# Performance work log

Hardware: AMD Instinct MI355X
Metric: run time of the kernel (lower is better)

The kernel has to match this reference:

```python
import jax, jax.numpy as jnp
import numpy as np

KEEP_RATIO = 0.7  # fully-annealed keep ratio (epoch >= 2*warmup_epochs)


def setup_inputs() -> dict:
    key = jax.random.key(0)
    k0, k1, k2 = jax.random.split(key, 3)
    B, H, W, C, HID = 16, 128, 128, 256, 128
    N = H * W
    tokens = jax.random.normal(k0, (B, N, C), dtype=jnp.float32)
    # xavier_uniform-ish init for the scorer MLP
    lim1 = float(np.sqrt(6.0 / (C + HID)))
    lim2 = float(np.sqrt(6.0 / (HID + 1)))
    w1 = jax.random.uniform(k1, (C, HID), minval=-lim1, maxval=lim1, dtype=jnp.float32)
    b1 = jnp.zeros((HID,), dtype=jnp.float32)
    w2 = jax.random.uniform(k2, (HID, 1), minval=-lim2, maxval=lim2, dtype=jnp.float32)
    b2 = jnp.zeros((1,), dtype=jnp.float32)
    return {"tokens": tokens, "w1": w1, "b1": b1, "w2": w2, "b2": b2}


def reference(tokens, w1, b1, w2, b2):
    # tokens: [B, N, C]; importance scorer: fc1 -> GELU(exact) -> fc2 -> squeeze
    B, N, C = tokens.shape
    num_keep = int(N * KEEP_RATIO)  # static; min_tokens=10 << num_keep
    h = jax.nn.gelu(jnp.einsum("bnc,ch->bnh", tokens, w1) + b1, approximate=False)
    scores = (jnp.einsum("bnh,ho->bno", h, w2) + b2)[..., 0]  # [B, N]
    # top-k token selection, then sort kept indices to preserve spatial order
    _, top_idx = jax.lax.top_k(scores, num_keep)          # [B, K]
    kept_indices = jnp.sort(top_idx, axis=-1)              # [B, K]
    pruned_tokens = jnp.take_along_axis(tokens, kept_indices[..., None], axis=1)  # [B, K, C]
    return pruned_tokens, kept_indices, scores
```

## Files before the change

kernel.cpp:

```cpp
#include <hip/hip_runtime.h>
#include <math.h>

#define B_ 16
#define N_ 16384
#define C_ 256
#define H_ 128
#define K_ 11468
#define G_ ((B_ * N_) / 16)
#define GPB_ 16
#define NBLK_ (G_ / GPB_)

typedef __attribute__((ext_vector_type(8))) short s16x8;
typedef __attribute__((ext_vector_type(4))) float f32x4;
typedef __attribute__((ext_vector_type(4))) unsigned int u32x4;

__device__ __forceinline__ unsigned short f2bf(float f) {
  unsigned u = __builtin_bit_cast(unsigned, f);
  return (unsigned short)((u + 0x7FFFu + ((u >> 16) & 1u)) >> 16);
}
__device__ __forceinline__ unsigned fkey(float f) {
  unsigned u = __builtin_bit_cast(unsigned, f);
  return (u & 0x80000000u) ? ~u : (u | 0x80000000u);
}
__device__ __forceinline__ unsigned pk2(float hi, float lo) {
  return __builtin_amdgcn_perm(__builtin_bit_cast(unsigned, hi),
                               __builtin_bit_cast(unsigned, lo), 0x07060302u);
}

#define LDS_BARRIER()                                     \
  do {                                                    \
    asm volatile("s_waitcnt lgkmcnt(0)" ::: "memory");    \
    __builtin_amdgcn_s_barrier();                         \
  } while (0)

__device__ __forceinline__ float gelu_fast(float h) {
  const float t = 0.5f * h * h;
  const float u = 0.147f * t;
  const float num = t * (1.2732395f + u);
  const float den = 1.0f + u;
  const float r = num * __builtin_amdgcn_rcpf(den);
  const float e = __builtin_amdgcn_exp2f(r * -1.44269504f);
  const float s = __builtin_amdgcn_sqrtf(fmaxf(1.0f - e, 0.0f));
  const unsigned sgn = __builtin_bit_cast(unsigned, h) & 0x80000000u;
  const float erfv = __builtin_bit_cast(float, __builtin_bit_cast(unsigned, s) | sgn);
  return 0.5f * h * (1.0f + erfv);
}

__global__ void k_prep(const float* __restrict__ w1, unsigned short* __restrict__ w1t) {
  int i = blockIdx.x * blockDim.x + threadIdx.x;
  if (i < C_ * H_) {
    int c = i / H_, h = i % H_;
    w1t[h * C_ + c] = f2bf(w1[i]);
  }
}

__global__ __launch_bounds__(256) void k_score(
    const float* __restrict__ tokens, const unsigned short* __restrict__ w1t,
    const float* __restrict__ b1, const float* __restrict__ w2,
    const float* __restrict__ b2, float* __restrict__ scores_out) {
  __shared__ unsigned short lds_a[2][8 * 64 * 8];
  __shared__ float lds_c[4][16];

  const int tid = threadIdx.x;
  const int lane = tid & 63;
  const int l15 = lane & 15;
  const int l4 = lane >> 4;
  const int w = tid >> 6;

  s16x8 bfr0[8], bfr1[8];
  const int row0 = (2 * w) * 16 + l15;
  const int row1 = row0 + 16;
#pragma unroll
  for (int kk = 0; kk < 8; ++kk) {
    bfr0[kk] = *reinterpret_cast<const s16x8*>(w1t + row0 * 256 + (l4 + 4 * kk) * 8);
    bfr1[kk] = *reinterpret_cast<const s16x8*>(w1t + row1 * 256 + (l4 + 4 * kk) * 8);
  }
  const float b1v0 = b1[row0], b1v1 = b1[row1];
  const float w2v0 = w2[row0], w2v1 = w2[row1];
  const float b2v = b2[0];

  const int t = tid & 15;
  const int s = tid >> 4;
  const int g0 = blockIdx.x * GPB_;
  const float* tg = tokens + ((size_t)(g0 * 16 + t)) * 256 + s * 16;
  const int lb0 = (2 * s) * 128 + t * 8;
  const int lb1 = lb0 + 128;

  f32x4 vv[4];

  {
#pragma unroll
    for (int q = 0; q < 4; ++q) vv[q] = *reinterpret_cast<const f32x4*>(tg + 4 * q);
    u32x4 o0, o1;
    o0[0] = pk2(vv[0][1], vv[0][0]);
    o0[1] = pk2(vv[0][3], vv[0][2]);
    o0[2] = pk2(vv[1][1], vv[1][0]);
    o0[3] = pk2(vv[1][3], vv[1][2]);
    o1[0] = pk2(vv[2][1], vv[2][0]);
    o1[1] = pk2(vv[2][3], vv[2][2]);
    o1[2] = pk2(vv[3][1], vv[3][0]);
    o1[3] = pk2(vv[3][3], vv[3][2]);
    *reinterpret_cast<u32x4*>(&lds_a[0][lb0]) = o0;
    *reinterpret_cast<u32x4*>(&lds_a[0][lb1]) = o1;
  }
  LDS_BARRIER();

  int cur = 0;
  for (int i = 0; i < GPB_; ++i) {
    const int g = g0 + i;
    if (i + 1 < GPB_) {
      const float* p = tg + (size_t)(i + 1) * 4096;
#pragma unroll
      for (int q = 0; q < 4; ++q) vv[q] = *reinterpret_cast<const f32x4*>(p + 4 * q);
    }

    f32x4 acc0 = (f32x4){0.f, 0.f, 0.f, 0.f};
    f32x4 acc1 = (f32x4){0.f, 0.f, 0.f, 0.f};
#pragma unroll
    for (int kk = 0; kk < 8; ++kk) {
      s16x8 a = *reinterpret_cast<const s16x8*>(&lds_a[cur][(kk * 64 + lane) * 8]);
      acc0 = __builtin_amdgcn_mfma_f32_16x16x32_bf16(a, bfr0[kk], acc0, 0, 0, 0);
      acc1 = __builtin_amdgcn_mfma_f32_16x16x32_bf16(a, bfr1[kk], acc1, 0, 0, 0);
    }

    float p4[4];
#pragma unroll
    for (int rr = 0; rr < 4; ++rr) {
      float sp = gelu_fast(acc0[rr] + b1v0) * w2v0 + gelu_fast(acc1[rr] + b1v1) * w2v1;
      sp += __shfl_xor(sp, 1);
      sp += __shfl_xor(sp, 2);
      sp += __shfl_xor(sp, 4);
      sp += __shfl_xor(sp, 8);
      p4[rr] = sp;
    }
    if (l15 == 0) {
#pragma unroll
      for (int rr = 0; rr < 4; ++rr) lds_c[w][l4 * 4 + rr] = p4[rr];
    }
    LDS_BARRIER();

    if (tid < 16) {
      scores_out[g * 16 + tid] =
          lds_c[0][tid] + lds_c[1][tid] + lds_c[2][tid] + lds_c[3][tid] + b2v;
    }
    if (i + 1 < GPB_) {
      u32x4 o0, o1;
      o0[0] = pk2(vv[0][1], vv[0][0]);
      o0[1] = pk2(vv[0][3], vv[0][2]);
      o0[2] = pk2(vv[1][1], vv[1][0]);
      o0[3] = pk2(vv[1][3], vv[1][2]);
      o1[0] = pk2(vv[2][1], vv[2][0]);
      o1[1] = pk2(vv[2][3], vv[2][2]);
      o1[2] = pk2(vv[3][1], vv[3][0]);
      o1[3] = pk2(vv[3][3], vv[3][2]);
      *reinterpret_cast<u32x4*>(&lds_a[cur ^ 1][lb0]) = o0;
      *reinterpret_cast<u32x4*>(&lds_a[cur ^ 1][lb1]) = o1;
    }
    LDS_BARRIER();
    cur ^= 1;
  }
}

__device__ unsigned block_exscan_1024(unsigned v, volatile unsigned* wsum) {
  const int lane = threadIdx.x & 63;
  const int w = threadIdx.x >> 6;
  unsigned x = v;
#pragma unroll
  for (int d = 1; d < 64; d <<= 1) {
    unsigned t = __shfl_up(x, d);
    if (lane >= d) x += t;
  }
  if (lane == 63) wsum[w] = x;
  __syncthreads();
  if (threadIdx.x == 0) {
    unsigned s = 0;
    for (int i = 0; i < 16; ++i) {
      unsigned t = wsum[i];
      wsum[i] = s;
      s += t;
    }
  }
  __syncthreads();
  unsigned r = wsum[w] + x - v;
  __syncthreads();
  return r;
}

__global__ __launch_bounds__(1024) void k_select(const float* __restrict__ scores_f,
                                                 int* __restrict__ kept,
                                                 float* __restrict__ out_idx) {
  __shared__ unsigned hist[256];
  __shared__ unsigned wsum[16];
  __shared__ unsigned sh_prefix, sh_rk;
  const int b = blockIdx.x;
  const int tid = threadIdx.x;
  const float* sp = scores_f + (size_t)b * N_;

  unsigned prefix = 0;
  unsigned rk = K_;
  for (int pass = 0; pass < 4; ++pass) {
    const int shift = 24 - pass * 8;
    if (tid < 256) hist[tid] = 0;
    __syncthreads();
    const unsigned pmask = pass ? (0xFFFFFFFFu << (shift + 8)) : 0u;
    for (int i = tid; i < N_; i += 1024) {
      unsigned k = fkey(sp[i]);
      if ((k & pmask) == prefix) atomicAdd(&hist[(k >> shift) & 255u], 1u);
    }
    __syncthreads();
    unsigned h = (tid < 256) ? hist[255 - tid] : 0u;
    unsigned s = block_exscan_1024(h, wsum);
    if (tid < 256 && s < rk && s + h >= rk) {
      sh_prefix = prefix | ((unsigned)(255 - tid) << shift);
      sh_rk = rk - s;
    }
    __syncthreads();
    prefix = sh_prefix;
    rk = sh_rk;
    __syncthreads();
  }
  const unsigned Tkey = prefix;
  const unsigned need = rk;

  const int i0 = tid * 16;
  unsigned neq = 0;
  for (int j = 0; j < 16; ++j) {
    unsigned k = fkey(sp[i0 + j]);
    neq += (k == Tkey);
  }
  unsigned eq_base = block_exscan_1024(neq, wsum);

  unsigned kcnt = 0;
  {
    unsigned eqr = eq_base;
    for (int j = 0; j < 16; ++j) {
      unsigned k = fkey(sp[i0 + j]);
      bool kp = (k > Tkey) || ((k == Tkey) && (eqr < need));
      eqr += (k == Tkey);
      kcnt += kp;
    }
  }
  unsigned pos = block_exscan_1024(kcnt, wsum);
  {
    unsigned eqr = eq_base;
    for (int j = 0; j < 16; ++j) {
      unsigned k = fkey(sp[i0 + j]);
      bool kp = (k > Tkey) || ((k == Tkey) && (eqr < need));
      eqr += (k == Tkey);
      if (kp) {
        kept[(size_t)b * K_ + pos] = i0 + j;
        out_idx[(size_t)b * K_ + pos] = (float)(i0 + j);
        ++pos;
      }
    }
  }
}

__global__ __launch_bounds__(256) void k_gather(const float* __restrict__ tokens,
                                                const int* __restrict__ kept,
                                                float* __restrict__ outp) {
  const int wid = (blockIdx.x * blockDim.x + threadIdx.x) >> 6;
  const int lane = threadIdx.x & 63;
  if (wid >= B_ * K_) return;
  const int b = wid / K_;
  const int idx = kept[wid];
  const f32x4 v = *reinterpret_cast<const f32x4*>(tokens + ((size_t)b * N_ + idx) * C_ + lane * 4);
  *reinterpret_cast<f32x4*>(outp + (size_t)wid * C_ + lane * 4) = v;
}

extern "C" void kernel_launch(void* const* d_in, const int* in_sizes, int n_in,
                              void* d_out, int out_size, void* d_ws, size_t ws_size,
                              hipStream_t stream) {
  const float* tokens = (const float*)d_in[0];
  const float* w1 = (const float*)d_in[1];
  const float* b1 = (const float*)d_in[2];
  const float* w2 = (const float*)d_in[3];
  const float* b2 = (const float*)d_in[4];

  float* out = (float*)d_out;
  float* out_pruned = out;
  float* out_idx = out + (size_t)B_ * K_ * C_;
  float* out_scores = out_idx + (size_t)B_ * K_;

  char* ws = (char*)d_ws;
  unsigned short* w1t = (unsigned short*)ws;
  int* kept = (int*)(ws + 0x10000);

  k_prep<<<dim3((C_ * H_ + 255) / 256), dim3(256), 0, stream>>>(w1, w1t);
  k_score<<<dim3(NBLK_), dim3(256), 0, stream>>>(tokens, w1t, b1, w2, b2, out_scores);
  k_select<<<dim3(B_), dim3(1024), 0, stream>>>(out_scores, kept, out_idx);
  k_gather<<<dim3((B_ * K_ + 3) / 4), dim3(256), 0, stream>>>(tokens, kept, out_pruned);
}
```

Measured before the change: 169.3 us.

## Use 11/11/10-bit radix select and a single packed scan for compaction

Replaces the four 8-bit radix passes in top-k selection with three passes over 11, 11 and 10 bits, each using a 2048- or 1024-bin histogram. The final compaction combines the greater-than and equal counts into one packed prefix scan, replacing two scans and three sweeps over the scores. The block scan now combines per-wave sums with a parallel shuffle across 16 lanes instead of a serial loop on one thread. Together these cut barriers and passes over scores in the select kernel, at the cost of a larger histogram and 16-bit packing limits in the scan.

```diff
diff --git a/kernel.cpp b/kernel.cpp
--- a/kernel.cpp
+++ b/kernel.cpp
@@ -87,7 +87,6 @@
   const int lb1 = lb0 + 128;
 
   f32x4 vv[4];
-
   {
 #pragma unroll
     for (int q = 0; q < 4; ++q) vv[q] = *reinterpret_cast<const f32x4*>(tg + 4 * q);
@@ -162,8 +161,9 @@
 }
 
 __device__ unsigned block_exscan_1024(unsigned v, volatile unsigned* wsum) {
-  const int lane = threadIdx.x & 63;
-  const int w = threadIdx.x >> 6;
+  const int tid = threadIdx.x;
+  const int lane = tid & 63;
+  const int w = tid >> 6;
   unsigned x = v;
 #pragma unroll
   for (int d = 1; d < 64; d <<= 1) {
@@ -172,16 +172,17 @@
   }
   if (lane == 63) wsum[w] = x;
   __syncthreads();
-  if (threadIdx.x == 0) {
-    unsigned s = 0;
-    for (int i = 0; i < 16; ++i) {
-      unsigned t = wsum[i];
-      wsum[i] = s;
-      s += t;
-    }
-  }
-  __syncthreads();
-  unsigned r = wsum[w] + x - v;
+  if (tid < 16) {
+    unsigned s = wsum[tid];
+#pragma unroll
+    for (int d = 1; d < 16; d <<= 1) {
+      unsigned u = __shfl_up(s, d);
+      if (tid >= d) s += u;
+    }
+    wsum[tid] = s;
+  }
+  __syncthreads();
+  unsigned r = (w ? wsum[w - 1] : 0u) + x - v;
   __syncthreads();
   return r;
 }
@@ -189,69 +190,90 @@
 __global__ __launch_bounds__(1024) void k_select(const float* __restrict__ scores_f,
                                                  int* __restrict__ kept,
                                                  float* __restrict__ out_idx) {
-  __shared__ unsigned hist[256];
+  __shared__ unsigned hist[2048];
   __shared__ unsigned wsum[16];
-  __shared__ unsigned sh_prefix, sh_rk;
+  __shared__ unsigned sh_T, sh_need;
   const int b = blockIdx.x;
   const int tid = threadIdx.x;
   const float* sp = scores_f + (size_t)b * N_;
 
-  unsigned prefix = 0;
-  unsigned rk = K_;
-  for (int pass = 0; pass < 4; ++pass) {
-    const int shift = 24 - pass * 8;
-    if (tid < 256) hist[tid] = 0;
-    __syncthreads();
-    const unsigned pmask = pass ? (0xFFFFFFFFu << (shift + 8)) : 0u;
-    for (int i = tid; i < N_; i += 1024) {
-      unsigned k = fkey(sp[i]);
-      if ((k & pmask) == prefix) atomicAdd(&hist[(k >> shift) & 255u], 1u);
-    }
-    __syncthreads();
-    unsigned h = (tid < 256) ? hist[255 - tid] : 0u;
-    unsigned s = block_exscan_1024(h, wsum);
-    if (tid < 256 && s < rk && s + h >= rk) {
-      sh_prefix = prefix | ((unsigned)(255 - tid) << shift);
-      sh_rk = rk - s;
-    }
-    __syncthreads();
-    prefix = sh_prefix;
-    rk = sh_rk;
-    __syncthreads();
-  }
-  const unsigned Tkey = prefix;
-  const unsigned need = rk;
+  hist[tid] = 0; hist[tid + 1024] = 0;
+  __syncthreads();
+  for (int i = tid; i < N_; i += 1024) atomicAdd(&hist[fkey(sp[i]) >> 21], 1u);
+  __syncthreads();
+  {
+    const int hi = 2047 - 2 * tid, lo = hi - 1;
+    const unsigned chi = hist[hi], pair = chi + hist[lo];
+    unsigned before = block_exscan_1024(pair, wsum);
+    if (before < K_ && before + chi >= K_) { sh_T = (unsigned)hi; sh_need = K_ - before; }
+    else if (before + chi < K_ && before + pair >= K_) { sh_T = (unsigned)lo; sh_need = K_ - before - chi; }
+  }
+  __syncthreads();
+  const unsigned T0 = sh_T;
+  unsigned needK = sh_need;
+  __syncthreads();
+
+  hist[tid] = 0; hist[tid + 1024] = 0;
+  __syncthreads();
+  for (int i = tid; i < N_; i += 1024) {
+    unsigned k = fkey(sp[i]);
+    if ((k >> 21) == T0) atomicAdd(&hist[(k >> 10) & 2047u], 1u);
+  }
+  __syncthreads();
+  {
+    const int hi = 2047 - 2 * tid, lo = hi - 1;
+    const unsigned chi = hist[hi], pair = chi + hist[lo];
+    unsigned before = block_exscan_1024(pair, wsum);
+    if (before < needK && before + chi >= needK) { sh_T = (unsigned)hi; sh_need = needK - before; }
+    else if (before + chi < needK && before + pair >= needK) { sh_T = (unsigned)lo; sh_need = needK - before - chi; }
+  }
+  __syncthreads();
+  const unsigned P21 = (T0 << 11) | sh_T;
+  needK = sh_need;
+  __syncthreads();
+
+  hist[tid] = 0;
+  __syncthreads();
+  for (int i = tid; i < N_; i += 1024) {
+    unsigned k = fkey(sp[i]);
+    if ((k >> 10) == P21) atomicAdd(&hist[k & 1023u], 1u);
+  }
+  __syncthreads();
+  {
+    const int hi = 1023 - tid;
+    const unsigned chi = hist[hi];
+    unsigned before = block_exscan_1024(chi, wsum);
+    if (before < needK && before + chi >= needK) { sh_T = (unsigned)hi; sh_need = needK - before; }
+  }
+  __syncthreads();
+  const unsigned Tkey = (P21 << 10) | sh_T;
+  const unsigned need = sh_need;
+  __syncthreads();
 
   const int i0 = tid * 16;
-  unsigned neq = 0;
+  unsigned cgt = 0, ceq = 0;
   for (int j = 0; j < 16; ++j) {
     unsigned k = fkey(sp[i0 + j]);
-    neq += (k == Tkey);
-  }
-  unsigned eq_base = block_exscan_1024(neq, wsum);
-
-  unsigned kcnt = 0;
-  {
-    unsigned eqr = eq_base;
-    for (int j = 0; j < 16; ++j) {
-      unsigned k = fkey(sp[i0 + j]);
-      bool kp = (k > Tkey) || ((k == Tkey) && (eqr < need));
-      eqr += (k == Tkey);
-      kcnt += kp;
-    }
-  }
-  unsigned pos = block_exscan_1024(kcnt, wsum);
-  {
-    unsigned eqr = eq_base;
-    for (int j = 0; j < 16; ++j) {
-      unsigned k = fkey(sp[i0 + j]);
-      bool kp = (k > Tkey) || ((k == Tkey) && (eqr < need));
-      eqr += (k == Tkey);
-      if (kp) {
+    cgt += (k > Tkey);
+    ceq += (k == Tkey);
+  }
+  unsigned packed = block_exscan_1024((cgt << 16) | ceq, wsum);
+  unsigned gt_b = packed >> 16;
+  unsigned eq_b = packed & 0xFFFFu;
+  for (int j = 0; j < 16; ++j) {
+    unsigned k = fkey(sp[i0 + j]);
+    if (k > Tkey) {
+      unsigned pos = gt_b + (eq_b < need ? eq_b : need);
+      kept[(size_t)b * K_ + pos] = i0 + j;
+      out_idx[(size_t)b * K_ + pos] = (float)(i0 + j);
+      ++gt_b;
+    } else if (k == Tkey) {
+      if (eq_b < need) {
+        unsigned pos = gt_b + eq_b;
         kept[(size_t)b * K_ + pos] = i0 + j;
         out_idx[(size_t)b * K_ + pos] = (float)(i0 + j);
-        ++pos;
       }
+      ++eq_b;
     }
   }
 }
```

After: 159.2 us, median of 2. -6.0%, faster.
